# Kernel tuning notes

Measured on AMD Instinct MI355X. Metric: run time of the kernel, lower is better.

The kernel has to match this reference:

```python
import jax, jax.numpy as jnp
import numpy as np

WIN = (2, 2, 8, 8)
NUM_HEADS = 6
DIM = 120
HID = int(DIM * 2.0)
SHAPE = (8, 4, 64, 64, DIM)


def _layernorm(x, w, b, eps=1e-5):
    m = jnp.mean(x, axis=-1, keepdims=True)
    v = jnp.mean((x - m) ** 2, axis=-1, keepdims=True)
    return (x - m) / jnp.sqrt(v + eps) * w + b


def _window_partition(x, win):
    N, D, H, W, C = x.shape
    x = x.reshape(N // win[0], win[0], D // win[1], win[1],
                  H // win[2], win[2], W // win[3], win[3], C)
    x = jnp.transpose(x, (0, 2, 4, 6, 1, 3, 5, 7, 8))
    return x.reshape(-1, win[0] * win[1] * win[2] * win[3], C)


def _window_reverse(wins, win, N, D, H, W):
    x = wins.reshape(N // win[0], D // win[1], H // win[2], W // win[3],
                     win[0], win[1], win[2], win[3], -1)
    x = jnp.transpose(x, (0, 4, 1, 5, 2, 6, 3, 7, 8))
    return x.reshape(N, D, H, W, -1)


def _mha(q, k, v, scale):
    # q,k,v: (B_, h, n, hd) -> (B_, n, h*hd)
    a = jax.nn.softmax(jnp.einsum('bhid,bhjd->bhij', q * scale, k), axis=-1)
    o = jnp.einsum('bhij,bhjd->bhid', a, v)
    B, h, n, hd = o.shape
    return jnp.transpose(o, (0, 2, 1, 3)).reshape(B, n, h * hd)


def _qkv(xw, W, b, heads):
    B, n, C = xw.shape
    qkv = (xw @ W.T + b).reshape(B, n, 3, heads, C // heads)
    qkv = jnp.transpose(qkv, (2, 0, 3, 1, 4))
    return qkv[0], qkv[1], qkv[2]


def _tmsa(x, norm1_w, norm1_b, qkv_self_w, qkv_self_b, qkv_mut_w, qkv_mut_b,
          proj_w, proj_b, norm2_w, norm2_b, fc11_w, fc11_b, fc12_w, fc12_b,
          fc2_w, fc2_b):
    N, D, H, W, C = x.shape
    heads = NUM_HEADS
    scale = (C // heads) ** -0.5
    # --- attention branch (no shift -> no roll, no mask; dims divide window -> no pad) ---
    h = _layernorm(x, norm1_w, norm1_b)
    xw = _window_partition(h, WIN)                       # (B_, n, C)
    q, k, v = _qkv(xw, qkv_self_w, qkv_self_b, heads)
    x_self = _mha(q, k, v, scale)                        # (B_, n, C)
    q, k, v = _qkv(xw, qkv_mut_w, qkv_mut_b, heads)
    n = xw.shape[1]
    q1, q2 = q[:, :, :n // 2], q[:, :, n // 2:]
    k1, k2 = k[:, :, :n // 2], k[:, :, n // 2:]
    v1, v2 = v[:, :, :n // 2], v[:, :, n // 2:]
    x1 = _mha(q2, k1, v1, scale)                         # (B_, n/2, C)
    x2 = _mha(q1, k2, v2, scale)
    x_mut = jnp.concatenate([x1, x2], axis=1)            # (B_, n, C)
    x_out = jnp.concatenate([x_mut, x_self], axis=2)     # (B_, n, 2C)
    attn = x_out @ proj_w.T + proj_b                     # (B_, n, C)
    attn = _window_reverse(attn, WIN, N, D, H, W)
    x = x + attn
    # --- GEGLU MLP branch ---
    h2 = _layernorm(x, norm2_w, norm2_b)
    gate = jax.nn.gelu(h2 @ fc11_w.T + fc11_b, approximate=False)
    hid = gate * (h2 @ fc12_w.T + fc12_b)
    x = x + (hid @ fc2_w.T + fc2_b)
    return x


def setup_inputs() -> dict:
    key = jax.random.key(0)
    ks = jax.random.split(key, 8)
    s = 0.02
    return {
        'x': jax.random.normal(ks[0], SHAPE, dtype=jnp.float32),
        'norm1_w': jnp.ones((DIM,), jnp.float32),
        'norm1_b': jnp.zeros((DIM,), jnp.float32),
        'qkv_self_w': jax.random.normal(ks[1], (3 * DIM, DIM), jnp.float32) * s,
        'qkv_self_b': jnp.zeros((3 * DIM,), jnp.float32),
        'qkv_mut_w': jax.random.normal(ks[2], (3 * DIM, DIM), jnp.float32) * s,
        'qkv_mut_b': jnp.zeros((3 * DIM,), jnp.float32),
        'proj_w': jax.random.normal(ks[3], (DIM, 2 * DIM), jnp.float32) * s,
        'proj_b': jnp.zeros((DIM,), jnp.float32),
        'norm2_w': jnp.ones((DIM,), jnp.float32),
        'norm2_b': jnp.zeros((DIM,), jnp.float32),
        'fc11_w': jax.random.normal(ks[4], (HID, DIM), jnp.float32) * s,
        'fc11_b': jnp.zeros((HID,), jnp.float32),
        'fc12_w': jax.random.normal(ks[5], (HID, DIM), jnp.float32) * s,
        'fc12_b': jnp.zeros((HID,), jnp.float32),
        'fc2_w': jax.random.normal(ks[6], (DIM, HID), jnp.float32) * s,
        'fc2_b': jnp.zeros((DIM,), jnp.float32),
    }


def reference(x, norm1_w, norm1_b, qkv_self_w, qkv_self_b, qkv_mut_w,
              qkv_mut_b, proj_w, proj_b, norm2_w, norm2_b, fc11_w, fc11_b,
              fc12_w, fc12_b, fc2_w, fc2_b):
    return _tmsa(x, norm1_w, norm1_b, qkv_self_w, qkv_self_b, qkv_mut_w,
                 qkv_mut_b, proj_w, proj_b, norm2_w, norm2_b, fc11_w, fc11_b,
                 fc12_w, fc12_b, fc2_w, fc2_b)
```

## Files before the change

kernel.cpp:

```cpp
#include <hip/hip_runtime.h>
#include <hip/hip_bf16.h>
#include <math.h>


typedef __attribute__((ext_vector_type(8))) short bf16x8;
typedef __attribute__((ext_vector_type(4))) float f32x4;

#define SCALE2 (0.22360679774997896f * 1.44269504088896340f)
#define CHROWS 65536
#define QPLANE 7864320u

union B8U { bf16x8 v; uint4 u4; uint2 u2[2]; unsigned u[4]; short s[8]; };

__device__ __forceinline__ short bf16b(float f) {
    __hip_bfloat16 h = __float2bfloat16(f);
    return *reinterpret_cast<short*>(&h);
}
__device__ __forceinline__ float bf2f(short s) {
    return __uint_as_float(((unsigned)(unsigned short)s) << 16);
}
__device__ __forceinline__ unsigned packbf(float a, float b) {
    return (unsigned)(unsigned short)bf16b(a) |
           ((unsigned)(unsigned short)bf16b(b) << 16);
}

__device__ __forceinline__ int rev_row(int r) {
    int w = r >> 8, t = r & 255;
    int w8 = w & 7, h8 = (w >> 3) & 7, d2 = (w >> 6) & 1, n2 = w >> 7;
    int www = t & 7, hh = (t >> 3) & 7, dd = (t >> 6) & 1, nn = t >> 7;
    int n = n2 * 2 + nn, d = d2 * 2 + dd;
    int Hc = h8 * 8 + hh, Wc = w8 * 8 + www;
    return ((n * 4 + d) << 12) + (Hc << 6) + Wc;
}
__device__ __forceinline__ int part_row(int g) {
    int ww = g & 63, hh = (g >> 6) & 63, d = (g >> 12) & 3, n = g >> 14;
    int w = ((n >> 1) * 2 + (d >> 1)) * 64 + ((hh >> 3) << 3) + (ww >> 3);
    int t = (((n & 1) * 2 + (d & 1)) << 6) + ((hh & 7) << 3) + (ww & 7);
    return (w << 8) + t;
}
__device__ __forceinline__ float gelu_exact(float x) {
    return 0.5f * x * (1.0f + erff(x * 0.70710678118654752f));
}

__device__ __forceinline__ bf16x8 load_frag20(const short* row, int quad) {
    B8U r;
    const uint2* p = (const uint2*)(row + quad * 8);
    r.u2[0] = p[0]; r.u2[1] = p[1];
    if (quad == 2) { r.u[2] = 0; r.u[3] = 0; }
    else if (quad == 3) { r.u[0] = r.u[1] = r.u[2] = r.u[3] = 0; }
    return r.v;
}

template <bool REMAP>
__global__ __launch_bounds__(256) void ln_kernel(const float* __restrict__ in,
                                                 const float* __restrict__ w,
                                                 const float* __restrict__ b,
                                                 short* __restrict__ out) {
    int row  = blockIdx.x * 4 + (threadIdx.x >> 6);
    int lane = threadIdx.x & 63;
    const float* xr = in + (size_t)row * 120;
    float2 v = make_float2(0.f, 0.f);
    if (lane < 60) v = *(const float2*)(xr + lane * 2);
    float s = v.x + v.y;
#pragma unroll
    for (int off = 32; off; off >>= 1) s += __shfl_down(s, off, 64);
    s = __shfl(s, 0, 64);
    float mean = s * (1.f / 120.f);
    float dx = v.x - mean, dy = v.y - mean;
    float q = (lane < 60) ? (dx * dx + dy * dy) : 0.f;
#pragma unroll
    for (int off = 32; off; off >>= 1) q += __shfl_down(q, off, 64);
    q = __shfl(q, 0, 64);
    float rstd = rsqrtf(q * (1.f / 120.f) + 1e-5f);
    int orow = REMAP ? part_row(row) : row;
    if (lane < 60) {
        float2 wv = *(const float2*)(w + lane * 2);
        float2 bv = *(const float2*)(b + lane * 2);
        unsigned u = packbf(dx * rstd * wv.x + bv.x, dy * rstd * wv.y + bv.y);
        *(unsigned*)(out + (size_t)orow * 120 + lane * 2) = u;
    }
}

template <int MODE, int K, int N>
__global__ __launch_bounds__(256) void mm(const short* __restrict__ A,
                                          const float* __restrict__ W,
                                          const float* __restrict__ bias,
                                          void* __restrict__ outp,
                                          const float* __restrict__ aux,
                                          int m0) {
    const int lane = threadIdx.x & 63, wave = threadIdx.x >> 6;
    const int quad = lane >> 4, l16 = lane & 15;
    const int bm = blockIdx.x * 128 + (wave >> 1) * 64;
    const int bn = blockIdx.y * 64 + (wave & 1) * 32;

    f32x4 acc[4][2];
#pragma unroll
    for (int i = 0; i < 4; ++i)
#pragma unroll
        for (int j = 0; j < 2; ++j) acc[i][j] = (f32x4){0.f, 0.f, 0.f, 0.f};

    const short* Ar[4];
#pragma unroll
    for (int i = 0; i < 4; ++i) Ar[i] = A + (size_t)(bm + i * 16 + l16) * K;
    const int n0 = bn + l16, n1 = bn + 16 + l16;
    const int nc0 = n0 < N ? n0 : N - 1;
    const int nc1 = n1 < N ? n1 : N - 1;
    const float* W0 = W + (size_t)nc0 * K;
    const float* W1 = W + (size_t)nc1 * K;

    const int KT = (K + 31) / 32;
#pragma unroll
    for (int kt = 0; kt < KT; ++kt) {
        int kk = kt * 32 + quad * 8;
        bool kok = kk < K;
        int kc = kok ? kk : 0;
        bf16x8 a[4], b0v, b1v;
#pragma unroll
        for (int i = 0; i < 4; ++i) a[i] = *(const bf16x8*)(Ar[i] + kc);
        {
            f32x4 w0 = *(const f32x4*)(W0 + kc);
            f32x4 w1 = *(const f32x4*)(W0 + kc + 4);
            b0v = (bf16x8){bf16b(w0.x), bf16b(w0.y), bf16b(w0.z), bf16b(w0.w),
                           bf16b(w1.x), bf16b(w1.y), bf16b(w1.z), bf16b(w1.w)};
            f32x4 w2 = *(const f32x4*)(W1 + kc);
            f32x4 w3 = *(const f32x4*)(W1 + kc + 4);
            b1v = (bf16x8){bf16b(w2.x), bf16b(w2.y), bf16b(w2.z), bf16b(w2.w),
                           bf16b(w3.x), bf16b(w3.y), bf16b(w3.z), bf16b(w3.w)};
        }
        if (!kok) {
            bf16x8 zz = {0, 0, 0, 0, 0, 0, 0, 0};
            a[0] = a[1] = a[2] = a[3] = b0v = b1v = zz;
        }
#pragma unroll
        for (int i = 0; i < 4; ++i) {
            acc[i][0] = __builtin_amdgcn_mfma_f32_16x16x32_bf16(a[i], b0v, acc[i][0], 0, 0, 0);
            acc[i][1] = __builtin_amdgcn_mfma_f32_16x16x32_bf16(a[i], b1v, acc[i][1], 0, 0, 0);
        }
    }

#pragma unroll
    for (int j = 0; j < 2; ++j) {
        const int n = j ? n1 : n0;
        if (n >= N) continue;
        const float bs = bias[n];
        int which = 0, head = 0, e = 0;
        if (MODE == 0) { which = n / 120; int hn = n % 120; head = hn / 20; e = hn % 20; }
#pragma unroll
        for (int i = 0; i < 4; ++i) {
#pragma unroll
            for (int r = 0; r < 4; ++r) {
                int m = bm + i * 16 + quad * 4 + r;
                float val = acc[i][j][r] + bs;
                if (MODE == 0) {
                    if (which == 0) val *= SCALE2;
                    int wl = m >> 8, t = m & 255;
                    ((short*)outp)[(size_t)which * QPLANE +
                                   ((size_t)((wl * 6 + head) * 256 + t)) * 20 + e] = bf16b(val);
                } else if (MODE == 1) {
                    int g = rev_row(m0 + m);
                    val += aux[(size_t)g * 120 + n];
                    ((float*)outp)[(size_t)(m0 + m) * 120 + n] = val;
                } else if (MODE == 2) {
                    ((short*)outp)[(size_t)m * 240 + n] = bf16b(gelu_exact(val));
                } else if (MODE == 3) {
                    size_t idx = (size_t)m * 240 + n;
                    short* o = (short*)outp;
                    o[idx] = bf16b(bf2f(o[idx]) * val);
                } else {
                    int g = rev_row(m0 + m);
                    val += aux[(size_t)m * 120 + n];
                    ((float*)outp)[(size_t)g * 120 + n] = val;
                }
            }
        }
    }
}

__global__ __launch_bounds__(256) void mm_mlp(const short* __restrict__ A,
                                              const float* __restrict__ W1,
                                              const float* __restrict__ b1,
                                              const float* __restrict__ W2,
                                              const float* __restrict__ b2,
                                              short* __restrict__ outp) {
    const int lane = threadIdx.x & 63, wave = threadIdx.x >> 6;
    const int quad = lane >> 4, l16 = lane & 15;
    const int bm = blockIdx.x * 128 + (wave >> 1) * 64;
    const int bn = blockIdx.y * 64 + (wave & 1) * 32;
    const int N = 240, K = 120;

    f32x4 acc1[4][2], acc2[4][2];
#pragma unroll
    for (int i = 0; i < 4; ++i)
#pragma unroll
        for (int j = 0; j < 2; ++j) {
            acc1[i][j] = (f32x4){0.f, 0.f, 0.f, 0.f};
            acc2[i][j] = (f32x4){0.f, 0.f, 0.f, 0.f};
        }

    const short* Ar[4];
#pragma unroll
    for (int i = 0; i < 4; ++i) Ar[i] = A + (size_t)(bm + i * 16 + l16) * K;
    const int n0 = bn + l16, n1 = bn + 16 + l16;
    const int nc0 = n0 < N ? n0 : N - 1;
    const int nc1 = n1 < N ? n1 : N - 1;
    const float* Wa0 = W1 + (size_t)nc0 * K;
    const float* Wa1 = W1 + (size_t)nc1 * K;
    const float* Wb0 = W2 + (size_t)nc0 * K;
    const float* Wb1 = W2 + (size_t)nc1 * K;

#pragma unroll
    for (int kt = 0; kt < 4; ++kt) {
        int kk = kt * 32 + quad * 8;
        bool kok = kk < K;
        int kc = kok ? kk : 0;
        bf16x8 a[4], p0v, p1v, q0v, q1v;
#pragma unroll
        for (int i = 0; i < 4; ++i) a[i] = *(const bf16x8*)(Ar[i] + kc);
        {
            f32x4 w0 = *(const f32x4*)(Wa0 + kc);
            f32x4 w1 = *(const f32x4*)(Wa0 + kc + 4);
            p0v = (bf16x8){bf16b(w0.x), bf16b(w0.y), bf16b(w0.z), bf16b(w0.w),
                           bf16b(w1.x), bf16b(w1.y), bf16b(w1.z), bf16b(w1.w)};
            f32x4 w2 = *(const f32x4*)(Wa1 + kc);
            f32x4 w3 = *(const f32x4*)(Wa1 + kc + 4);
            p1v = (bf16x8){bf16b(w2.x), bf16b(w2.y), bf16b(w2.z), bf16b(w2.w),
                           bf16b(w3.x), bf16b(w3.y), bf16b(w3.z), bf16b(w3.w)};
            f32x4 u0 = *(const f32x4*)(Wb0 + kc);
            f32x4 u1 = *(const f32x4*)(Wb0 + kc + 4);
            q0v = (bf16x8){bf16b(u0.x), bf16b(u0.y), bf16b(u0.z), bf16b(u0.w),
                           bf16b(u1.x), bf16b(u1.y), bf16b(u1.z), bf16b(u1.w)};
            f32x4 u2 = *(const f32x4*)(Wb1 + kc);
            f32x4 u3 = *(const f32x4*)(Wb1 + kc + 4);
            q1v = (bf16x8){bf16b(u2.x), bf16b(u2.y), bf16b(u2.z), bf16b(u2.w),
                           bf16b(u3.x), bf16b(u3.y), bf16b(u3.z), bf16b(u3.w)};
        }
        if (!kok) {
            bf16x8 zz = {0, 0, 0, 0, 0, 0, 0, 0};
            a[0] = a[1] = a[2] = a[3] = p0v = p1v = q0v = q1v = zz;
        }
#pragma unroll
        for (int i = 0; i < 4; ++i) {
            acc1[i][0] = __builtin_amdgcn_mfma_f32_16x16x32_bf16(a[i], p0v, acc1[i][0], 0, 0, 0);
            acc1[i][1] = __builtin_amdgcn_mfma_f32_16x16x32_bf16(a[i], p1v, acc1[i][1], 0, 0, 0);
            acc2[i][0] = __builtin_amdgcn_mfma_f32_16x16x32_bf16(a[i], q0v, acc2[i][0], 0, 0, 0);
            acc2[i][1] = __builtin_amdgcn_mfma_f32_16x16x32_bf16(a[i], q1v, acc2[i][1], 0, 0, 0);
        }
    }

#pragma unroll
    for (int j = 0; j < 2; ++j) {
        const int n = j ? n1 : n0;
        if (n >= N) continue;
        const float g1 = b1[n], g2 = b2[n];
#pragma unroll
        for (int i = 0; i < 4; ++i) {
#pragma unroll
            for (int r = 0; r < 4; ++r) {
                int m = bm + i * 16 + quad * 4 + r;
                float gv = acc1[i][j][r] + g1;
                float vv = acc2[i][j][r] + g2;
                outp[(size_t)m * 240 + n] = bf16b(gelu_exact(gv) * vv);
            }
        }
    }
}

template <int NK, bool MUT>
__global__ __launch_bounds__(NK) void attn_flash(const short* __restrict__ qkv,
                                                 short* __restrict__ xout) {
    constexpr int NKT = NK / 32;
    constexpr int VSTR2 = NK + 4;
    __shared__ __align__(16) short Kf[NKT * 2 * 48 * 8];
    __shared__ __align__(16) unsigned Vt2[11 * VSTR2];
    const int b = blockIdx.x;
    int wl, hd, half;
    if (MUT) { half = b & 1; hd = (b >> 1) % 6; wl = b / 12; }
    else     { half = 0;     hd = b % 6;        wl = b / 6;  }
    const int tid  = threadIdx.x;
    const int lane = tid & 63, wave = tid >> 6;
    const int quad = lane >> 4, l16 = lane & 15;

    const size_t rb = (size_t)(wl * 6 + hd) * 256;
    const short* qpl = qkv + rb * 20;
    const short* kpl = qkv + (size_t)QPLANE + rb * 20;
    const short* vpl = qkv + 2 * (size_t)QPLANE + rb * 20;
    const int koff = MUT ? half * 128 : 0;
    const int qoff = MUT ? (1 - half) * 128 : 0;

    {
        const uint2* p = (const uint2*)(vpl + (size_t)(koff + tid) * 20);
        unsigned tmp[10];
#pragma unroll
        for (int i = 0; i < 5; ++i) ((uint2*)tmp)[i] = p[i];
#pragma unroll
        for (int i = 0; i < 10; ++i) Vt2[i * VSTR2 + tid] = tmp[i];
        Vt2[10 * VSTR2 + tid] = 0x00003F80u;

        int skt = tid >> 5, sf = (tid >> 4) & 1, sl = tid & 15;
        int srow = koff + skt * 32 + sf * 4 + ((sl >> 2) << 3) + (sl & 3);
        const uint2* kp = (const uint2*)(kpl + (size_t)srow * 20);
        uint2 k0 = kp[0], k1 = kp[1], k2 = kp[2], k3 = kp[3], k4 = kp[4];
        uint4* dst = (uint4*)Kf + ((skt * 2 + sf) * 48 + sl);
        dst[0]  = make_uint4(k0.x, k0.y, k1.x, k1.y);
        dst[16] = make_uint4(k2.x, k2.y, k3.x, k3.y);
        dst[32] = make_uint4(k4.x, k4.y, 0u, 0u);
    }
    __syncthreads();

    const int quadc = quad < 3 ? quad : 2;
    const uint4* kfrag = (const uint4*)Kf + quadc * 16 + l16;
    const unsigned sel = (l16 & 1) ? 0x07060302u : 0x05040100u;
    const unsigned* vbase0 = Vt2 + (l16 >> 1) * VSTR2;
    int r1 = 8 + (l16 >> 1); if (r1 > 10) r1 = 10;
    const unsigned* vbase1 = Vt2 + r1 * VSTR2;
    const f32x4 z4 = {0.f, 0.f, 0.f, 0.f};

#pragma unroll 1
    for (int g = 0; g < 2; ++g) {
        bf16x8 bq0 = load_frag20(qpl + (size_t)(qoff + wave * 64 + (g * 2 + 0) * 16 + l16) * 20, quad);
        bf16x8 bq1 = load_frag20(qpl + (size_t)(qoff + wave * 64 + (g * 2 + 1) * 16 + l16) * 20, quad);

        f32x4 accO[2][2];
        accO[0][0] = z4; accO[0][1] = z4; accO[1][0] = z4; accO[1][1] = z4;

#pragma unroll
        for (int kt = 0; kt < NKT; ++kt) {
            B8U ak0, ak1;
            ak0.u4 = kfrag[(kt * 2 + 0) * 48];
            ak1.u4 = kfrag[(kt * 2 + 1) * 48];
            B8U av0, av1;
            {
                uint4 va = *(const uint4*)(vbase0 + kt * 32 + quad * 8);
                uint4 vb = *(const uint4*)(vbase0 + kt * 32 + quad * 8 + 4);
                av0.u[0] = __builtin_amdgcn_perm(va.y, va.x, sel);
                av0.u[1] = __builtin_amdgcn_perm(va.w, va.z, sel);
                av0.u[2] = __builtin_amdgcn_perm(vb.y, vb.x, sel);
                av0.u[3] = __builtin_amdgcn_perm(vb.w, vb.z, sel);
                uint4 vc = *(const uint4*)(vbase1 + kt * 32 + quad * 8);
                uint4 vd = *(const uint4*)(vbase1 + kt * 32 + quad * 8 + 4);
                av1.u[0] = __builtin_amdgcn_perm(vc.y, vc.x, sel);
                av1.u[1] = __builtin_amdgcn_perm(vc.w, vc.z, sel);
                av1.u[2] = __builtin_amdgcn_perm(vd.y, vd.x, sel);
                av1.u[3] = __builtin_amdgcn_perm(vd.w, vd.z, sel);
            }
#pragma unroll
            for (int t = 0; t < 2; ++t) {
                bf16x8 bqt = t ? bq1 : bq0;
                f32x4 s0 = __builtin_amdgcn_mfma_f32_16x16x32_bf16(ak0.v, bqt, z4, 0, 0, 0);
                f32x4 s1 = __builtin_amdgcn_mfma_f32_16x16x32_bf16(ak1.v, bqt, z4, 0, 0, 0);
                float p0 = __builtin_amdgcn_exp2f(s0[0]), p1 = __builtin_amdgcn_exp2f(s0[1]);
                float p2 = __builtin_amdgcn_exp2f(s0[2]), p3 = __builtin_amdgcn_exp2f(s0[3]);
                float p4 = __builtin_amdgcn_exp2f(s1[0]), p5 = __builtin_amdgcn_exp2f(s1[1]);
                float p6 = __builtin_amdgcn_exp2f(s1[2]), p7 = __builtin_amdgcn_exp2f(s1[3]);
                B8U bp;
                bp.u[0] = packbf(p0, p1);
                bp.u[1] = packbf(p2, p3);
                bp.u[2] = packbf(p4, p5);
                bp.u[3] = packbf(p6, p7);
                accO[t][0] = __builtin_amdgcn_mfma_f32_16x16x32_bf16(av0.v, bp.v, accO[t][0], 0, 0, 0);
                accO[t][1] = __builtin_amdgcn_mfma_f32_16x16x32_bf16(av1.v, bp.v, accO[t][1], 0, 0, 0);
            }
        }

#pragma unroll
        for (int t = 0; t < 2; ++t) {
            int nt = g * 2 + t;
            float l = __shfl(accO[t][1][0], 16 + l16, 64);
            float inv = 1.f / l;
            int tok = (MUT ? half * 128 : 0) + wave * 64 + nt * 16 + l16;
            short* orow = xout + (size_t)(wl * 256 + tok) * 240 + (MUT ? hd * 20 : 120 + hd * 20);
            unsigned lo = packbf(accO[t][0][0] * inv, accO[t][0][1] * inv);
            unsigned hi2 = packbf(accO[t][0][2] * inv, accO[t][0][3] * inv);
            *(uint2*)(orow + quad * 4) = make_uint2(lo, hi2);
            if (quad == 0) {
                unsigned lo2 = packbf(accO[t][1][0] * inv, accO[t][1][1] * inv);
                unsigned hi3 = packbf(accO[t][1][2] * inv, accO[t][1][3] * inv);
                *(uint2*)(orow + 16) = make_uint2(lo2, hi3);
            }
        }
    }
}

extern "C" void kernel_launch(void* const* d_in, const int* in_sizes, int n_in,
                              void* d_out, int out_size, void* d_ws, size_t ws_size,
                              hipStream_t stream) {
    const float* x          = (const float*)d_in[0];
    const float* norm1_w    = (const float*)d_in[1];
    const float* norm1_b    = (const float*)d_in[2];
    const float* qkv_self_w = (const float*)d_in[3];
    const float* qkv_self_b = (const float*)d_in[4];
    const float* qkv_mut_w  = (const float*)d_in[5];
    const float* qkv_mut_b  = (const float*)d_in[6];
    const float* proj_w     = (const float*)d_in[7];
    const float* proj_b     = (const float*)d_in[8];
    const float* norm2_w    = (const float*)d_in[9];
    const float* norm2_b    = (const float*)d_in[10];
    const float* fc11_w     = (const float*)d_in[11];
    const float* fc11_b     = (const float*)d_in[12];
    const float* fc12_w     = (const float*)d_in[13];
    const float* fc12_b     = (const float*)d_in[14];
    const float* fc2_w      = (const float*)d_in[15];
    const float* fc2_b      = (const float*)d_in[16];

    if (ws_size < 110100480u) return;

    char* wsb   = (char*)d_ws;
    short* Hb    = (short*)wsb;
    short* QKVc  = (short*)(wsb + 31457280);
    short* XOUTc = (short*)(wsb + 78643200);
    float* TMP   = (float*)wsb;
    short* H2c   = (short*)(wsb + 62914560);
    short* HIDc  = (short*)(wsb + 78643200);
    float* X2    = (float*)d_out;
    float* out   = (float*)d_out;

    ln_kernel<true><<<32768, 256, 0, stream>>>(x, norm1_w, norm1_b, Hb);

    for (int c = 0; c < 2; ++c) {
        int m0 = c * CHROWS;
        const short* Ac = Hb + (size_t)m0 * 120;
        mm<0, 120, 360><<<dim3(512, 6), 256, 0, stream>>>(Ac, qkv_self_w, qkv_self_b,
                                                          QKVc, nullptr, 0);
        attn_flash<256, false><<<1536, 256, 0, stream>>>(QKVc, XOUTc);
        mm<0, 120, 360><<<dim3(512, 6), 256, 0, stream>>>(Ac, qkv_mut_w, qkv_mut_b,
                                                          QKVc, nullptr, 0);
        attn_flash<128, true><<<3072, 128, 0, stream>>>(QKVc, XOUTc);
        mm<1, 240, 120><<<dim3(512, 2), 256, 0, stream>>>(XOUTc, proj_w, proj_b,
                                                          X2, x, m0);
    }

    hipMemcpyAsync(TMP, d_out, 62914560u, hipMemcpyDeviceToDevice, stream);

    for (int c = 0; c < 2; ++c) {
        int m0 = c * CHROWS;
        ln_kernel<false><<<16384, 256, 0, stream>>>(TMP + (size_t)m0 * 120,
                                                    norm2_w, norm2_b, H2c);
        mm_mlp<<<dim3(512, 4), 256, 0, stream>>>(H2c, fc11_w, fc11_b,
                                                 fc12_w, fc12_b, HIDc);
        mm<4, 240, 120><<<dim3(512, 2), 256, 0, stream>>>(HIDc, fc2_w, fc2_b,
                                                          out, TMP + (size_t)m0 * 120, m0);
    }
}
```

Before: 672.0 us.

## Stage GEMM A and weight tiles through padded LDS with bf16 conversion

The mm and mm_mlp kernels now cooperatively load the 128-row A tile and the 64-row weight tile (converted to bf16) into padded shared memory, then feed the MFMAs from LDS instead of per-wave global loads. This removes redundant global reads and repeated fp32-to-bf16 conversion across waves. The K tail is zero-padded in shared memory, and the unused MODE 2/3 epilogues are dropped. It adds LDS usage, which may limit occupancy, plus a barrier per K phase. The staging assumes K is a multiple of 120.

```diff
diff --git a/kernel.cpp b/kernel.cpp
--- a/kernel.cpp
+++ b/kernel.cpp
@@ -9,6 +9,7 @@
 #define SCALE2 (0.22360679774997896f * 1.44269504088896340f)
 #define CHROWS 65536
 #define QPLANE 7864320u
+#define KPAD 136
 
 union B8U { bf16x8 v; uint4 u4; uint2 u2[2]; unsigned u[4]; short s[8]; };
 
@@ -49,6 +50,35 @@
     if (quad == 2) { r.u[2] = 0; r.u[3] = 0; }
     else if (quad == 3) { r.u[0] = r.u[1] = r.u[2] = r.u[3] = 0; }
     return r.v;
+}
+
+__device__ __forceinline__ void stage_A(short* As, const short* __restrict__ A,
+                                        int bm, int k0, int Astr, int tid) {
+#pragma unroll
+    for (int i = 0; i < 8; ++i) {
+        int c = tid + i * 256;
+        if (c < 1920) {
+            int row = c / 15, slot = c - row * 15;
+            uint4 v = *(const uint4*)(A + (size_t)(bm + row) * Astr + k0 + slot * 8);
+            *(uint4*)(As + row * KPAD + slot * 8) = v;
+        }
+    }
+    if (tid < 128) *(uint4*)(As + tid * KPAD + 120) = make_uint4(0u, 0u, 0u, 0u);
+}
+__device__ __forceinline__ void stage_W(short* Ws, const float* __restrict__ W,
+                                        int bn, int k0, int Wstr, int N, int tid) {
+#pragma unroll
+    for (int i = 0; i < 8; ++i) {
+        int c = tid + i * 256;
+        if (c < 1920) {
+            int row = c / 30, slot = c - row * 30;
+            int wr = bn + row; if (wr > N - 1) wr = N - 1;
+            f32x4 v = *(const f32x4*)(W + (size_t)wr * Wstr + k0 + slot * 4);
+            *(uint2*)(Ws + row * KPAD + slot * 4) = make_uint2(packbf(v.x, v.y),
+                                                               packbf(v.z, v.w));
+        }
+    }
+    if (tid < 64) *(uint4*)(Ws + tid * KPAD + 120) = make_uint4(0u, 0u, 0u, 0u);
 }
 
 template <bool REMAP>
@@ -88,10 +118,15 @@
                                           void* __restrict__ outp,
                                           const float* __restrict__ aux,
                                           int m0) {
-    const int lane = threadIdx.x & 63, wave = threadIdx.x >> 6;
+    __shared__ __align__(16) short As[128 * KPAD];
+    __shared__ __align__(16) short Ws[64 * KPAD];
+    const int tid = threadIdx.x;
+    const int lane = tid & 63, wave = tid >> 6;
     const int quad = lane >> 4, l16 = lane & 15;
-    const int bm = blockIdx.x * 128 + (wave >> 1) * 64;
-    const int bn = blockIdx.y * 64 + (wave & 1) * 32;
+    const int bmb = blockIdx.x * 128;
+    const int bn  = blockIdx.y * 64;
+    const int abase = (wave >> 1) * 64;
+    const int wbase = (wave & 1) * 32;
 
     f32x4 acc[4][2];
 #pragma unroll
@@ -99,48 +134,32 @@
 #pragma unroll
         for (int j = 0; j < 2; ++j) acc[i][j] = (f32x4){0.f, 0.f, 0.f, 0.f};
 
-    const short* Ar[4];
-#pragma unroll
-    for (int i = 0; i < 4; ++i) Ar[i] = A + (size_t)(bm + i * 16 + l16) * K;
-    const int n0 = bn + l16, n1 = bn + 16 + l16;
-    const int nc0 = n0 < N ? n0 : N - 1;
-    const int nc1 = n1 < N ? n1 : N - 1;
-    const float* W0 = W + (size_t)nc0 * K;
-    const float* W1 = W + (size_t)nc1 * K;
-
-    const int KT = (K + 31) / 32;
-#pragma unroll
-    for (int kt = 0; kt < KT; ++kt) {
-        int kk = kt * 32 + quad * 8;
-        bool kok = kk < K;
-        int kc = kok ? kk : 0;
-        bf16x8 a[4], b0v, b1v;
-#pragma unroll
-        for (int i = 0; i < 4; ++i) a[i] = *(const bf16x8*)(Ar[i] + kc);
-        {
-            f32x4 w0 = *(const f32x4*)(W0 + kc);
-            f32x4 w1 = *(const f32x4*)(W0 + kc + 4);
-            b0v = (bf16x8){bf16b(w0.x), bf16b(w0.y), bf16b(w0.z), bf16b(w0.w),
-                           bf16b(w1.x), bf16b(w1.y), bf16b(w1.z), bf16b(w1.w)};
-            f32x4 w2 = *(const f32x4*)(W1 + kc);
-            f32x4 w3 = *(const f32x4*)(W1 + kc + 4);
-            b1v = (bf16x8){bf16b(w2.x), bf16b(w2.y), bf16b(w2.z), bf16b(w2.w),
-                           bf16b(w3.x), bf16b(w3.y), bf16b(w3.z), bf16b(w3.w)};
-        }
-        if (!kok) {
-            bf16x8 zz = {0, 0, 0, 0, 0, 0, 0, 0};
-            a[0] = a[1] = a[2] = a[3] = b0v = b1v = zz;
-        }
-#pragma unroll
-        for (int i = 0; i < 4; ++i) {
-            acc[i][0] = __builtin_amdgcn_mfma_f32_16x16x32_bf16(a[i], b0v, acc[i][0], 0, 0, 0);
-            acc[i][1] = __builtin_amdgcn_mfma_f32_16x16x32_bf16(a[i], b1v, acc[i][1], 0, 0, 0);
-        }
-    }
-
+    constexpr int PH = K / 120;
+#pragma unroll
+    for (int p = 0; p < PH; ++p) {
+        if (p) __syncthreads();
+        stage_A(As, A, bmb, p * 120, K, tid);
+        stage_W(Ws, W, bn, p * 120, K, N, tid);
+        __syncthreads();
+        const short* Ab = As + (abase + l16) * KPAD + quad * 8;
+        const short* Wb = Ws + (wbase + l16) * KPAD + quad * 8;
+#pragma unroll
+        for (int kt = 0; kt < 4; ++kt) {
+            bf16x8 b0 = *(const bf16x8*)(Wb + kt * 32);
+            bf16x8 b1 = *(const bf16x8*)(Wb + 16 * KPAD + kt * 32);
+#pragma unroll
+            for (int i = 0; i < 4; ++i) {
+                bf16x8 a = *(const bf16x8*)(Ab + i * 16 * KPAD + kt * 32);
+                acc[i][0] = __builtin_amdgcn_mfma_f32_16x16x32_bf16(a, b0, acc[i][0], 0, 0, 0);
+                acc[i][1] = __builtin_amdgcn_mfma_f32_16x16x32_bf16(a, b1, acc[i][1], 0, 0, 0);
+            }
+        }
+    }
+
+    const int bm = bmb + abase;
 #pragma unroll
     for (int j = 0; j < 2; ++j) {
-        const int n = j ? n1 : n0;
+        const int n = bn + wbase + j * 16 + l16;
         if (n >= N) continue;
         const float bs = bias[n];
         int which = 0, head = 0, e = 0;
@@ -160,12 +179,6 @@
                     int g = rev_row(m0 + m);
                     val += aux[(size_t)g * 120 + n];
                     ((float*)outp)[(size_t)(m0 + m) * 120 + n] = val;
-                } else if (MODE == 2) {
-                    ((short*)outp)[(size_t)m * 240 + n] = bf16b(gelu_exact(val));
-                } else if (MODE == 3) {
-                    size_t idx = (size_t)m * 240 + n;
-                    short* o = (short*)outp;
-                    o[idx] = bf16b(bf2f(o[idx]) * val);
                 } else {
                     int g = rev_row(m0 + m);
                     val += aux[(size_t)m * 120 + n];
@@ -182,11 +195,17 @@
                                               const float* __restrict__ W2,
                                               const float* __restrict__ b2,
                                               short* __restrict__ outp) {
-    const int lane = threadIdx.x & 63, wave = threadIdx.x >> 6;
+    __shared__ __align__(16) short As[128 * KPAD];
+    __shared__ __align__(16) short Wa[64 * KPAD];
+    __shared__ __align__(16) short Wbs[64 * KPAD];
+    const int tid = threadIdx.x;
+    const int lane = tid & 63, wave = tid >> 6;
     const int quad = lane >> 4, l16 = lane & 15;
-    const int bm = blockIdx.x * 128 + (wave >> 1) * 64;
-    const int bn = blockIdx.y * 64 + (wave & 1) * 32;
-    const int N = 240, K = 120;
+    const int bmb = blockIdx.x * 128;
+    const int bn  = blockIdx.y * 64;
+    const int abase = (wave >> 1) * 64;
+    const int wbase = (wave & 1) * 32;
+    const int N = 240;
 
     f32x4 acc1[4][2], acc2[4][2];
 #pragma unroll
@@ -197,59 +216,33 @@
             acc2[i][j] = (f32x4){0.f, 0.f, 0.f, 0.f};
         }
 
-    const short* Ar[4];
-#pragma unroll
-    for (int i = 0; i < 4; ++i) Ar[i] = A + (size_t)(bm + i * 16 + l16) * K;
-    const int n0 = bn + l16, n1 = bn + 16 + l16;
-    const int nc0 = n0 < N ? n0 : N - 1;
-    const int nc1 = n1 < N ? n1 : N - 1;
-    const float* Wa0 = W1 + (size_t)nc0 * K;
-    const float* Wa1 = W1 + (size_t)nc1 * K;
-    const float* Wb0 = W2 + (size_t)nc0 * K;
-    const float* Wb1 = W2 + (size_t)nc1 * K;
-
+    stage_A(As, A, bmb, 0, 120, tid);
+    stage_W(Wa, W1, bn, 0, 120, N, tid);
+    stage_W(Wbs, W2, bn, 0, 120, N, tid);
+    __syncthreads();
+    const short* Ab  = As  + (abase + l16) * KPAD + quad * 8;
+    const short* W1b = Wa  + (wbase + l16) * KPAD + quad * 8;
+    const short* W2b = Wbs + (wbase + l16) * KPAD + quad * 8;
 #pragma unroll
     for (int kt = 0; kt < 4; ++kt) {
-        int kk = kt * 32 + quad * 8;
-        bool kok = kk < K;
-        int kc = kok ? kk : 0;
-        bf16x8 a[4], p0v, p1v, q0v, q1v;
-#pragma unroll
-        for (int i = 0; i < 4; ++i) a[i] = *(const bf16x8*)(Ar[i] + kc);
-        {
-            f32x4 w0 = *(const f32x4*)(Wa0 + kc);
-            f32x4 w1 = *(const f32x4*)(Wa0 + kc + 4);
-            p0v = (bf16x8){bf16b(w0.x), bf16b(w0.y), bf16b(w0.z), bf16b(w0.w),
-                           bf16b(w1.x), bf16b(w1.y), bf16b(w1.z), bf16b(w1.w)};
-            f32x4 w2 = *(const f32x4*)(Wa1 + kc);
-            f32x4 w3 = *(const f32x4*)(Wa1 + kc + 4);
-            p1v = (bf16x8){bf16b(w2.x), bf16b(w2.y), bf16b(w2.z), bf16b(w2.w),
-                           bf16b(w3.x), bf16b(w3.y), bf16b(w3.z), bf16b(w3.w)};
-            f32x4 u0 = *(const f32x4*)(Wb0 + kc);
-            f32x4 u1 = *(const f32x4*)(Wb0 + kc + 4);
-            q0v = (bf16x8){bf16b(u0.x), bf16b(u0.y), bf16b(u0.z), bf16b(u0.w),
-                           bf16b(u1.x), bf16b(u1.y), bf16b(u1.z), bf16b(u1.w)};
-            f32x4 u2 = *(const f32x4*)(Wb1 + kc);
-            f32x4 u3 = *(const f32x4*)(Wb1 + kc + 4);
-            q1v = (bf16x8){bf16b(u2.x), bf16b(u2.y), bf16b(u2.z), bf16b(u2.w),
-                           bf16b(u3.x), bf16b(u3.y), bf16b(u3.z), bf16b(u3.w)};
-        }
-        if (!kok) {
-            bf16x8 zz = {0, 0, 0, 0, 0, 0, 0, 0};
-            a[0] = a[1] = a[2] = a[3] = p0v = p1v = q0v = q1v = zz;
-        }
+        bf16x8 p0 = *(const bf16x8*)(W1b + kt * 32);
+        bf16x8 p1 = *(const bf16x8*)(W1b + 16 * KPAD + kt * 32);
+        bf16x8 q0 = *(const bf16x8*)(W2b + kt * 32);
+        bf16x8 q1 = *(const bf16x8*)(W2b + 16 * KPAD + kt * 32);
 #pragma unroll
         for (int i = 0; i < 4; ++i) {
-            acc1[i][0] = __builtin_amdgcn_mfma_f32_16x16x32_bf16(a[i], p0v, acc1[i][0], 0, 0, 0);
-            acc1[i][1] = __builtin_amdgcn_mfma_f32_16x16x32_bf16(a[i], p1v, acc1[i][1], 0, 0, 0);
-            acc2[i][0] = __builtin_amdgcn_mfma_f32_16x16x32_bf16(a[i], q0v, acc2[i][0], 0, 0, 0);
-            acc2[i][1] = __builtin_amdgcn_mfma_f32_16x16x32_bf16(a[i], q1v, acc2[i][1], 0, 0, 0);
-        }
-    }
-
+            bf16x8 a = *(const bf16x8*)(Ab + i * 16 * KPAD + kt * 32);
+            acc1[i][0] = __builtin_amdgcn_mfma_f32_16x16x32_bf16(a, p0, acc1[i][0], 0, 0, 0);
+            acc1[i][1] = __builtin_amdgcn_mfma_f32_16x16x32_bf16(a, p1, acc1[i][1], 0, 0, 0);
+            acc2[i][0] = __builtin_amdgcn_mfma_f32_16x16x32_bf16(a, q0, acc2[i][0], 0, 0, 0);
+            acc2[i][1] = __builtin_amdgcn_mfma_f32_16x16x32_bf16(a, q1, acc2[i][1], 0, 0, 0);
+        }
+    }
+
+    const int bm = bmb + abase;
 #pragma unroll
     for (int j = 0; j < 2; ++j) {
-        const int n = j ? n1 : n0;
+        const int n = bn + wbase + j * 16 + l16;
         if (n >= N) continue;
         const float g1 = b1[n], g2 = b2[n];
 #pragma unroll
```

Result: faster. 650.7 us (-3.2%).
